# Kernel tuning notes

Hardware: AMD Instinct MI355X
Metric: run time of the kernel (lower is better)

Reference implementation:

```python
import jax, jax.numpy as jnp
import numpy as np

N = 20000; E = 240000; F_IN = 128; EMB = 256; H = 2
G = 128; DENSE = 512; NCLS = 10; NL = 3; SLOPE = 0.2  # PyG GATConv default negative_slope

def setup_inputs() -> dict:
    key = jax.random.key(0)
    ks = jax.random.split(key, 64); it = iter(ks)
    def rn(shape, s=0.05):
        return jax.random.normal(next(it), shape, jnp.float32) * s
    inp = {}
    inp["x"] = jax.random.normal(next(it), (N, F_IN), jnp.float32)
    inp["edge_index"] = jax.random.randint(next(it), (2, E), 0, N)
    inp["batch_index"] = jnp.sort(jax.random.randint(next(it), (N,), 0, G))
    for i in range(NL):
        fin = F_IN if i == 0 else EMB
        inp[f"att_W{i}"] = rn((fin, H * EMB))
        inp[f"att_asrc{i}"] = rn((H, EMB))
        inp[f"att_adst{i}"] = rn((H, EMB))
        inp[f"att_b{i}"] = rn((H * EMB,))
        inp[f"lin_W{i}"] = rn((H * EMB, EMB))
        inp[f"lin_b{i}"] = rn((EMB,))
    inp["line1_W"] = rn((2 * EMB, DENSE))
    inp["line1_b"] = rn((DENSE,))
    inp["line2_W"] = rn((DENSE, NCLS))
    inp["line2_b"] = rn((NCLS,))
    return inp

def _gat_conv(x, src, dst, W, a_src, a_dst, b):
    # PyG GATConv, heads=2, concat=True, self-loops already in (src,dst)
    h = (x @ W).reshape(N, H, EMB)                     # [N,H,C]
    al_src = jnp.sum(h * a_src[None], -1)              # [N,H]
    al_dst = jnp.sum(h * a_dst[None], -1)              # [N,H]
    e = jax.nn.leaky_relu(al_src[src] + al_dst[dst], SLOPE)  # [Etot,H]
    m = jax.ops.segment_max(e, dst, num_segments=N)    # segment softmax over incoming edges
    ex = jnp.exp(e - m[dst])
    s = jax.ops.segment_sum(ex, dst, num_segments=N)
    alpha = ex / s[dst]
    out = jax.ops.segment_sum(h[src] * alpha[:, :, None], dst, num_segments=N)
    return out.reshape(N, H * EMB) + b

def _pool(x, batch_index):
    counts = jax.ops.segment_sum(jnp.ones((N,), x.dtype), batch_index, num_segments=G)
    mean = jax.ops.segment_sum(x, batch_index, num_segments=G) / jnp.maximum(counts, 1.0)[:, None]
    mx = jax.ops.segment_max(x, batch_index, num_segments=G)
    mx = jnp.where(counts[:, None] > 0, mx, 0.0)
    return jnp.concatenate([mx, mean], axis=1)         # [G, 2*EMB]

def _forward(x, edge_index, batch_index, params):
    loop = jnp.arange(N)
    src = jnp.concatenate([edge_index[0], loop])       # GATConv adds self-loops
    dst = jnp.concatenate([edge_index[1], loop])
    reps = []
    for i in range(NL):
        W, asrc, adst, b, lW, lb = params[i]
        x = jax.nn.relu(_gat_conv(x, src, dst, W, asrc, adst, b))
        x = jax.nn.relu(x @ lW + lb)
        reps.append(_pool(x, batch_index))
    g = reps[0] + reps[1] + reps[2]
    line1_W, line1_b, line2_W, line2_b = params[NL]
    g = jax.nn.relu(g @ line1_W + line1_b)
    # dropout is identity in eval mode
    return g @ line2_W + line2_b

def reference(x, edge_index, batch_index, att_W0, att_asrc0, att_adst0, att_b0, lin_W0, lin_b0, att_W1, att_asrc1, att_adst1, att_b1, lin_W1, lin_b1, att_W2, att_asrc2, att_adst2, att_b2, lin_W2, lin_b2, line1_W, line1_b, line2_W, line2_b):
    params = [
        (att_W0, att_asrc0, att_adst0, att_b0, lin_W0, lin_b0),
        (att_W1, att_asrc1, att_adst1, att_b1, lin_W1, lin_b1),
        (att_W2, att_asrc2, att_adst2, att_b2, lin_W2, lin_b2),
        (line1_W, line1_b, line2_W, line2_b),
    ]
    return _forward(x, edge_index, batch_index, params)
```

## Files before the change

### kernel.cpp

```cpp
#include <hip/hip_runtime.h>

#define Nn 20000
#define Ee 240000
#define ET (Ee + Nn)
#define EMB 256
#define HE  512
#define NG  128
#define DENSE 512
#define NCLS 10
#define SLOPE 0.2f
#define NB 79
#define PS 8

typedef unsigned short u16;
typedef short bf16x8 __attribute__((ext_vector_type(8)));
typedef float f32x4 __attribute__((ext_vector_type(4)));

__device__ __forceinline__ u16 f2bf(float f) {
    unsigned u = __float_as_uint(f);
    unsigned r = (u + 0x7fffu + ((u >> 16) & 1u)) >> 16;
    return (u16)r;
}
__device__ __forceinline__ float bf2f(u16 u) {
    return __uint_as_float(((unsigned)u) << 16);
}

__device__ __forceinline__ float wave_sum(float v) {
#pragma unroll
    for (int off = 32; off > 0; off >>= 1) v += __shfl_down(v, off, 64);
    return v;
}
__device__ __forceinline__ float block_sum4(float v, volatile float* red4) {
    v = wave_sum(v);
    if ((threadIdx.x & 63) == 0) red4[threadIdx.x >> 6] = v;
    __syncthreads();
    float r = red4[0] + red4[1] + red4[2] + red4[3];
    __syncthreads();
    return r;
}

__global__ __launch_bounds__(256) void conv_bf16_zero(const float* __restrict__ in, u16* __restrict__ out,
                                                      int n4, int* __restrict__ deg,
                                                      float* __restrict__ poolbuf) {
    if (blockIdx.x < NB) {
        int z = blockIdx.x * 256 + threadIdx.x;
        if (z < Nn) deg[z] = 0;
    }
    if (blockIdx.x >= 1000 && blockIdx.x < 1512) {
        int z = (blockIdx.x - 1000) * 256 + threadIdx.x;
        poolbuf[z] = 0.f;
    }
    int i = blockIdx.x * 256 + threadIdx.x;
    if (i >= n4) return;
    float4 v = ((const float4*)in)[i];
    ushort4 o;
    o.x = f2bf(v.x); o.y = f2bf(v.y); o.z = f2bf(v.z); o.w = f2bf(v.w);
    ((ushort4*)out)[i] = o;
}

struct PrepArgs {
    const float* attW[3]; const float* linW[3];
    const float* asrc[3]; const float* adst[3];
    u16* wt1[3]; u16* wt2[3]; float* wvec;
    int fin[3];
};

__global__ __launch_bounds__(256) void prep_weights(PrepArgs a) {
    __shared__ float tile[32][33];
    int task = blockIdx.y, bx = blockIdx.x, t = threadIdx.x;
    if (task < 3) {
        int i = task, K = a.fin[i];
        int nb = bx & 15, kb = bx >> 4;
        if (kb * 32 >= K) return;
        int n0 = nb * 32, k0 = kb * 32;
        int tx = t & 31, ty = t >> 5;
        const float* in = a.attW[i];
        u16* out = a.wt1[i];
#pragma unroll
        for (int j = 0; j < 32; j += 8) tile[ty + j][tx] = in[(size_t)(k0 + ty + j) * 512 + n0 + tx];
        __syncthreads();
#pragma unroll
        for (int j = 0; j < 32; j += 8) out[(size_t)(n0 + ty + j) * K + k0 + tx] = f2bf(tile[tx][ty + j]);
    } else if (task < 6) {
        int i = task - 3;
        int nb = bx & 7, kb = bx >> 3;
        if (kb >= 16) return;
        int n0 = nb * 32, k0 = kb * 32;
        int tx = t & 31, ty = t >> 5;
        const float* in = a.linW[i];
        u16* out = a.wt2[i];
#pragma unroll
        for (int j = 0; j < 32; j += 8) tile[ty + j][tx] = in[(size_t)(k0 + ty + j) * 256 + n0 + tx];
        __syncthreads();
#pragma unroll
        for (int j = 0; j < 32; j += 8) out[(size_t)(n0 + ty + j) * 512 + k0 + tx] = f2bf(tile[tx][ty + j]);
    } else {
        int i = task - 6, k = bx;
        if (k >= a.fin[i]) return;
        volatile float* red4 = &tile[0][0];
        const float* W = a.attW[i];
        float w0 = W[(size_t)k * HE + t];
        float w1 = W[(size_t)k * HE + EMB + t];
        float s0 = block_sum4(w0 * a.asrc[i][t], red4);
        float s1 = block_sum4(w1 * a.asrc[i][EMB + t], red4);
        float d0 = block_sum4(w0 * a.adst[i][t], red4);
        float d1 = block_sum4(w1 * a.adst[i][EMB + t], red4);
        if (t == 0) {
            float* wv = a.wvec + i * 1024 + k * 4;
            wv[0] = s0; wv[1] = s1; wv[2] = d0; wv[3] = d1;
        }
    }
}

__global__ __launch_bounds__(256) void edge_hist(const int* __restrict__ ei, int* __restrict__ deg) {
    int e = blockIdx.x * 256 + threadIdx.x;
    if (e >= ET) return;
    int d = (e < Ee) ? ei[Ee + e] : (e - Ee);
    atomicAdd(&deg[d], 1);
}

__global__ __launch_bounds__(256) void scan_blocks(const int* __restrict__ deg, int* __restrict__ incl,
                                                   int* __restrict__ bsum) {
    __shared__ int buf[256];
    int i = blockIdx.x * 256 + threadIdx.x;
    int v = (i < Nn) ? deg[i] : 0;
    buf[threadIdx.x] = v;
    __syncthreads();
    for (int off = 1; off < 256; off <<= 1) {
        int add = (threadIdx.x >= off) ? buf[threadIdx.x - off] : 0;
        __syncthreads();
        buf[threadIdx.x] += add;
        __syncthreads();
    }
    if (i < Nn) incl[i] = buf[threadIdx.x];
    if (threadIdx.x == 255) bsum[blockIdx.x] = buf[255];
}

__global__ __launch_bounds__(256) void scan_tops_groups(const int* __restrict__ bsum, int* __restrict__ boff,
                                                        const int* __restrict__ batch, int* __restrict__ gptr) {
    if (blockIdx.x == 0) {
        __shared__ int buf[128];
        int t = threadIdx.x;
        if (t < 128) buf[t] = (t < NB) ? bsum[t] : 0;
        __syncthreads();
        for (int off = 1; off < 128; off <<= 1) {
            int add = 0;
            if (t < 128 && t >= off) add = buf[t - off];
            __syncthreads();
            if (t < 128) buf[t] += add;
            __syncthreads();
        }
        if (t < NB) boff[t] = (t == 0) ? 0 : buf[t - 1];
    } else {
        int g = threadIdx.x;
        if (g > NG) return;
        int lo = 0, hi = Nn;
        while (lo < hi) {
            int mid = (lo + hi) >> 1;
            if (batch[mid] < g) lo = mid + 1; else hi = mid;
        }
        gptr[g] = lo;
    }
}

__global__ __launch_bounds__(256) void scan_add_cursor(const int* __restrict__ incl, const int* __restrict__ boff,
                                                       const int* __restrict__ deg, int* __restrict__ rowptr,
                                                       int* __restrict__ cursor) {
    int i = blockIdx.x * 256 + threadIdx.x;
    if (i < Nn) {
        int inc = incl[i] + boff[blockIdx.x];
        rowptr[i + 1] = inc;
        cursor[i] = inc - deg[i];
    }
    if (i == 0) rowptr[0] = 0;
}

__global__ __launch_bounds__(256) void edge_scatter(const int* __restrict__ ei, int* __restrict__ cursor,
                                                    int* __restrict__ colv) {
    int e = blockIdx.x * 256 + threadIdx.x;
    if (e >= ET) return;
    int s, d;
    if (e < Ee) { s = ei[e]; d = ei[Ee + e]; }
    else        { s = d = e - Ee; }
    int pos = atomicAdd(&cursor[d], 1);
    colv[pos] = s;
}

#define GL_LDS(gsrc, ldst)                                                               \
    __builtin_amdgcn_global_load_lds(                                                    \
        (const __attribute__((address_space(1))) void*)(unsigned long long)(gsrc),       \
        (__attribute__((address_space(3))) void*)(unsigned)(unsigned long long)(ldst),   \
        16, 0, 0)

__global__ __launch_bounds__(256) void gemm_bf16(const u16* __restrict__ A, int lda, int aoff,
                                                 const u16* __restrict__ Bt, const float* __restrict__ bias,
                                                 u16* __restrict__ Cb, int M, int N, int K, int relu) {
    __shared__ alignas(16) char sA[8192];
    __shared__ alignas(16) char sB[8192];
    int tid = threadIdx.x, lane = tid & 63, wid = tid >> 6;
    int l15 = lane & 15, q = lane >> 4;
    int row0 = blockIdx.y * 128, col0 = blockIdx.x * 128;
    int wrow = (wid >> 1) * 64, wcol = (wid & 1) * 64;
    int ao = (col0 >= 256) ? aoff : 0;

    f32x4 acc[4][4];
#pragma unroll
    for (int m = 0; m < 4; m++)
#pragma unroll
        for (int n = 0; n < 4; n++)
#pragma unroll
            for (int e = 0; e < 4; e++) acc[m][n][e] = 0.f;

    for (int k0 = 0; k0 < K; k0 += 32) {
#pragma unroll
        for (int is = 0; is < 2; ++is) {
            int base = is * 4096 + wid * 1024;
            int o = base + lane * 16;
            int row = o >> 6, kb = o & 63;
            int gr = row0 + row; gr = gr < M ? gr : M - 1;
            const char* src = (const char*)(A + (size_t)gr * lda + ao + k0) + kb;
            GL_LDS(src, sA + base);
        }
#pragma unroll
        for (int is = 0; is < 2; ++is) {
            int base = is * 4096 + wid * 1024;
            int o = base + lane * 16;
            int row = o >> 6, kb = o & 63;
            const char* src = (const char*)(Bt + (size_t)(col0 + row) * K + k0) + kb;
            GL_LDS(src, sB + base);
        }
        __syncthreads();

        bf16x8 af[4], bfr[4];
#pragma unroll
        for (int m = 0; m < 4; m++)
            af[m] = *(const bf16x8*)(sA + ((wrow + m * 16 + l15) << 6) + q * 16);
#pragma unroll
        for (int n = 0; n < 4; n++)
            bfr[n] = *(const bf16x8*)(sB + ((wcol + n * 16 + l15) << 6) + q * 16);
#pragma unroll
        for (int m = 0; m < 4; m++)
#pragma unroll
            for (int n = 0; n < 4; n++)
                acc[m][n] = __builtin_amdgcn_mfma_f32_16x16x32_bf16(af[m], bfr[n], acc[m][n], 0, 0, 0);
        __syncthreads();
    }

#pragma unroll
    for (int m = 0; m < 4; m++) {
        int rbase = row0 + wrow + m * 16 + q * 4;
#pragma unroll
        for (int reg = 0; reg < 4; reg++) {
            int r = rbase + reg;
            if (r >= M) continue;
#pragma unroll
            for (int n = 0; n < 4; n++) {
                int c = col0 + wcol + n * 16 + l15;
                float v = acc[m][n][reg] + (bias ? bias[c] : 0.f);
                if (relu) v = fmaxf(v, 0.f);
                Cb[(size_t)r * N + c] = f2bf(v);
            }
        }
    }
}

__global__ __launch_bounds__(256) void compute_al_fused(const u16* __restrict__ Xb, const float* __restrict__ wvec,
                                                        float* __restrict__ alsrc, float* __restrict__ aldst,
                                                        int fin) {
    int n = blockIdx.x * 4 + (threadIdx.x >> 6);
    int lane = threadIdx.x & 63;
    float s0 = 0.f, s1 = 0.f, d0 = 0.f, d1 = 0.f;
    for (int j = lane; j < fin; j += 64) {
        float x = bf2f(Xb[(size_t)n * fin + j]);
        float4 w = *(const float4*)(wvec + j * 4);
        s0 += x * w.x; s1 += x * w.y; d0 += x * w.z; d1 += x * w.w;
    }
#pragma unroll
    for (int off = 32; off > 0; off >>= 1) {
        s0 += __shfl_xor(s0, off, 64); s1 += __shfl_xor(s1, off, 64);
        d0 += __shfl_xor(d0, off, 64); d1 += __shfl_xor(d1, off, 64);
    }
    if (lane == 0) {
        alsrc[n * 2 + 0] = s0; alsrc[n * 2 + 1] = s1;
        aldst[n * 2 + 0] = d0; aldst[n * 2 + 1] = d1;
    }
}

__device__ __forceinline__ float lrelu(float x) { return x >= 0.f ? x : SLOPE * x; }

template <int FIN>
__global__ __launch_bounds__(256) void attn_agg_x(const u16* __restrict__ Xb,
                                                  const float* __restrict__ alsrc,
                                                  const float* __restrict__ aldst,
                                                  const int* __restrict__ row_ptr,
                                                  const int* __restrict__ colv,
                                                  u16* __restrict__ Zb) {
    constexpr int FPL = FIN / 64;
    int d = blockIdx.x * 4 + (threadIdx.x >> 6);
    int lane = threadIdx.x & 63;
    float ad0 = aldst[d * 2 + 0], ad1 = aldst[d * 2 + 1];
    int beg = row_ptr[d], end = row_ptr[d + 1];
    float S0 = 0.f, S1 = 0.f;
    float a0[FPL] = {}, a1[FPL] = {};

    int k = beg;
    for (; k + 3 < end; k += 4) {
        int ss[4];
        float e0[4], e1[4];
        u16 vv[4][FPL];
#pragma unroll
        for (int u = 0; u < 4; u++) ss[u] = colv[k + u];
#pragma unroll
        for (int u = 0; u < 4; u++) {
            float2 l = *(const float2*)(alsrc + ss[u] * 2);
            e0[u] = __expf(lrelu(l.x + ad0));
            e1[u] = __expf(lrelu(l.y + ad1));
            if constexpr (FPL == 4)
                *(ushort4*)vv[u] = *(const ushort4*)(Xb + (size_t)ss[u] * FIN + lane * 4);
            else
                *(ushort2*)vv[u] = *(const ushort2*)(Xb + (size_t)ss[u] * FIN + lane * 2);
        }
#pragma unroll
        for (int u = 0; u < 4; u++) {
            S0 += e0[u]; S1 += e1[u];
#pragma unroll
            for (int j = 0; j < FPL; j++) {
                float x = bf2f(vv[u][j]);
                a0[j] += e0[u] * x;
                a1[j] += e1[u] * x;
            }
        }
    }
    for (; k < end; ++k) {
        int s0 = colv[k];
        float2 l0 = *(const float2*)(alsrc + s0 * 2);
        float e00 = __expf(lrelu(l0.x + ad0)), e01 = __expf(lrelu(l0.y + ad1));
        u16 v0[FPL];
        if constexpr (FPL == 4) *(ushort4*)v0 = *(const ushort4*)(Xb + (size_t)s0 * FIN + lane * 4);
        else                    *(ushort2*)v0 = *(const ushort2*)(Xb + (size_t)s0 * FIN + lane * 2);
        S0 += e00; S1 += e01;
#pragma unroll
        for (int j = 0; j < FPL; j++) {
            float x0 = bf2f(v0[j]);
            a0[j] += e00 * x0;
            a1[j] += e01 * x0;
        }
    }

    float r0 = 1.f / S0, r1 = 1.f / S1;
    u16 o0[FPL], o1[FPL];
#pragma unroll
    for (int j = 0; j < FPL; j++) { o0[j] = f2bf(a0[j] * r0); o1[j] = f2bf(a1[j] * r1); }
    u16* q = Zb + (size_t)d * (2 * FIN);
    if constexpr (FPL == 4) {
        *(ushort4*)(q + lane * 4)       = *(ushort4*)o0;
        *(ushort4*)(q + FIN + lane * 4) = *(ushort4*)o1;
    } else {
        *(ushort2*)(q + lane * 2)       = *(ushort2*)o0;
        *(ushort2*)(q + FIN + lane * 2) = *(ushort2*)o1;
    }
}

__global__ __launch_bounds__(256) void pool_atomic(const u16* __restrict__ Xb, const int* __restrict__ gptr,
                                                   float* __restrict__ pmax, float* __restrict__ psum) {
    int g = blockIdx.x, sb = blockIdx.y, t = threadIdx.x;
    int beg = gptr[g], end = gptr[g + 1];
    float mx = 0.f, sm = 0.f;
    for (int n = beg + sb; n < end; n += PS) {
        float v = bf2f(Xb[(size_t)n * EMB + t]);
        mx = fmaxf(mx, v);
        sm += v;
    }
    atomicMax((int*)&pmax[g * EMB + t], __float_as_int(mx));
    atomicAdd(&psum[g * EMB + t], sm);
}

__global__ __launch_bounds__(256) void head1(const float* __restrict__ pmax3, const float* __restrict__ psum,
                                             const int* __restrict__ gptr,
                                             const float* __restrict__ l1W, const float* __restrict__ l1b,
                                             float* __restrict__ g1) {
    __shared__ float row[512];
    __shared__ float part[256];
    int r = blockIdx.y, t = threadIdx.x;
    for (int j = t; j < 512; j += 256) {
        float v;
        if (j < EMB) {
            v = pmax3[r * EMB + j] + pmax3[32768 + r * EMB + j] + pmax3[65536 + r * EMB + j];
        } else {
            int cnt = gptr[r + 1] - gptr[r];
            v = psum[r * EMB + (j - EMB)] / fmaxf((float)cnt, 1.f);
        }
        row[j] = v;
    }
    __syncthreads();
    int cl = t & 63, kq = t >> 6;
    int c = blockIdx.x * 64 + cl;
    int k0 = kq * 128;
    float acc = 0.f;
#pragma unroll 8
    for (int k = 0; k < 128; k++) acc += row[k0 + k] * l1W[(size_t)(k0 + k) * DENSE + c];
    part[t] = acc;
    __syncthreads();
    if (kq == 0) {
        float v = part[cl] + part[64 + cl] + part[128 + cl] + part[192 + cl];
        g1[(size_t)r * DENSE + c] = fmaxf(v + l1b[c], 0.f);
    }
}

__global__ __launch_bounds__(64) void line2_kernel(const float* __restrict__ g1, const float* __restrict__ W,
                                                   const float* __restrict__ b, float* __restrict__ out) {
    int r = blockIdx.x, t = threadIdx.x;
    float acc[NCLS] = {};
    for (int k = t; k < 2 * EMB; k += 64) {
        float gv = g1[r * 512 + k];
#pragma unroll
        for (int c = 0; c < NCLS; c++) acc[c] += gv * W[k * NCLS + c];
    }
#pragma unroll
    for (int c = 0; c < NCLS; c++) {
        float v = acc[c];
#pragma unroll
        for (int off = 32; off > 0; off >>= 1) v += __shfl_down(v, off, 64);
        if (t == 0) out[r * NCLS + c] = v + b[c];
    }
}

extern "C" void kernel_launch(void* const* d_in, const int* in_sizes, int n_in,
                              void* d_out, int out_size, void* d_ws, size_t ws_size,
                              hipStream_t stream) {
    const float* x_in  = (const float*)d_in[0];
    const int*   ei    = (const int*)d_in[1];
    const int*   batch = (const int*)d_in[2];
    const float* attW[3] = {(const float*)d_in[3],  (const float*)d_in[9],  (const float*)d_in[15]};
    const float* asrc[3] = {(const float*)d_in[4],  (const float*)d_in[10], (const float*)d_in[16]};
    const float* adst[3] = {(const float*)d_in[5],  (const float*)d_in[11], (const float*)d_in[17]};
    const float* attB[3] = {(const float*)d_in[6],  (const float*)d_in[12], (const float*)d_in[18]};
    const float* linW[3] = {(const float*)d_in[7],  (const float*)d_in[13], (const float*)d_in[19]};
    const float* linB[3] = {(const float*)d_in[8],  (const float*)d_in[14], (const float*)d_in[20]};
    const float* l1W = (const float*)d_in[21];
    const float* l1b = (const float*)d_in[22];
    const float* l2W = (const float*)d_in[23];
    const float* l2b = (const float*)d_in[24];
    float* out = (float*)d_out;

    char* ws = (char*)d_ws;
    size_t off = 0;
    auto alloc = [&](size_t bytes) -> void* {
        void* p = ws + off;
        off += (bytes + 255) & ~(size_t)255;
        return p;
    };
    u16*   Zb     = (u16*)alloc((size_t)Nn * HE * 2);
    u16*   Xb     = (u16*)alloc((size_t)Nn * EMB * 2);
    u16*   Yb     = (u16*)alloc((size_t)Nn * HE * 2);
    u16*   wt1[3], *wt2[3];
    for (int i = 0; i < 3; i++) {
        wt1[i] = (u16*)alloc((size_t)512 * 512 * 2);
        wt2[i] = (u16*)alloc((size_t)256 * 512 * 2);
    }
    float* wvec   = (float*)alloc((size_t)3 * 256 * 4 * 4);
    float* alsrc  = (float*)alloc((size_t)Nn * 2 * 4);
    float* aldst  = (float*)alloc((size_t)Nn * 2 * 4);
    int*   deg    = (int*)alloc((size_t)Nn * 4);
    int*   incl   = (int*)alloc((size_t)Nn * 4);
    int*   bsum   = (int*)alloc((size_t)NB * 4);
    int*   boff   = (int*)alloc((size_t)NB * 4);
    int*   rowptr = (int*)alloc((size_t)(Nn + 1) * 4);
    int*   cursor = (int*)alloc((size_t)Nn * 4);
    int*   colv   = (int*)alloc((size_t)ET * 4);
    int*   gptr   = (int*)alloc((size_t)(NG + 1) * 4);
    float* poolbuf = (float*)alloc((size_t)(3 * NG * EMB + NG * EMB) * 4);
    float* pmax3  = poolbuf;
    float* psumA  = poolbuf + 3 * NG * EMB;
    float* g1     = (float*)alloc((size_t)NG * DENSE * 4);

    conv_bf16_zero<<<(Nn * 128 / 4 + 255) / 256, 256, 0, stream>>>(x_in, Xb, Nn * 128 / 4, deg, poolbuf);

    PrepArgs pa;
    for (int i = 0; i < 3; i++) {
        pa.attW[i] = attW[i]; pa.linW[i] = linW[i];
        pa.asrc[i] = asrc[i]; pa.adst[i] = adst[i];
        pa.wt1[i] = wt1[i];   pa.wt2[i] = wt2[i];
        pa.fin[i] = (i == 0) ? 128 : EMB;
    }
    pa.wvec = wvec;
    prep_weights<<<dim3(256, 9), 256, 0, stream>>>(pa);

    edge_hist<<<(ET + 255) / 256, 256, 0, stream>>>(ei, deg);
    scan_blocks<<<NB, 256, 0, stream>>>(deg, incl, bsum);
    scan_tops_groups<<<2, 256, 0, stream>>>(bsum, boff, batch, gptr);
    scan_add_cursor<<<NB, 256, 0, stream>>>(incl, boff, deg, rowptr, cursor);
    edge_scatter<<<(ET + 255) / 256, 256, 0, stream>>>(ei, cursor, colv);

    for (int i = 0; i < 3; i++) {
        int fin = (i == 0) ? 128 : EMB;
        compute_al_fused<<<Nn / 4, 256, 0, stream>>>(Xb, wvec + i * 1024, alsrc, aldst, fin);
        if (fin == 128)
            attn_agg_x<128><<<Nn / 4, 256, 0, stream>>>(Xb, alsrc, aldst, rowptr, colv, Zb);
        else
            attn_agg_x<256><<<Nn / 4, 256, 0, stream>>>(Xb, alsrc, aldst, rowptr, colv, Zb);
        gemm_bf16<<<dim3(512 / 128, (Nn + 127) / 128), 256, 0, stream>>>(
            Zb, 2 * fin, fin, wt1[i], attB[i], Yb, Nn, 512, fin, 1);
        gemm_bf16<<<dim3(256 / 128, (Nn + 127) / 128), 256, 0, stream>>>(
            Yb, 512, 0, wt2[i], linB[i], Xb, Nn, 256, 512, 1);
        pool_atomic<<<dim3(NG, PS), 256, 0, stream>>>(Xb, gptr, pmax3 + i * NG * EMB, psumA);
    }

    head1<<<dim3(8, NG), 256, 0, stream>>>(pmax3, psumA, gptr, l1W, l1b, g1);
    line2_kernel<<<NG, 64, 0, stream>>>(g1, l2W, l2b, out);
}
```

Before: 420.0 us.

## Merge prologue kernels, fuse pooling with next-layer attention logits, deepen GEMM K-tile

```diff
diff --git a/kernel.cpp b/kernel.cpp
--- a/kernel.cpp
+++ b/kernel.cpp
@@ -39,25 +39,6 @@
     return r;
 }
 
-__global__ __launch_bounds__(256) void conv_bf16_zero(const float* __restrict__ in, u16* __restrict__ out,
-                                                      int n4, int* __restrict__ deg,
-                                                      float* __restrict__ poolbuf) {
-    if (blockIdx.x < NB) {
-        int z = blockIdx.x * 256 + threadIdx.x;
-        if (z < Nn) deg[z] = 0;
-    }
-    if (blockIdx.x >= 1000 && blockIdx.x < 1512) {
-        int z = (blockIdx.x - 1000) * 256 + threadIdx.x;
-        poolbuf[z] = 0.f;
-    }
-    int i = blockIdx.x * 256 + threadIdx.x;
-    if (i >= n4) return;
-    float4 v = ((const float4*)in)[i];
-    ushort4 o;
-    o.x = f2bf(v.x); o.y = f2bf(v.y); o.z = f2bf(v.z); o.w = f2bf(v.w);
-    ((ushort4*)out)[i] = o;
-}
-
 struct PrepArgs {
     const float* attW[3]; const float* linW[3];
     const float* asrc[3]; const float* adst[3];
@@ -65,10 +46,31 @@
     int fin[3];
 };
 
-__global__ __launch_bounds__(256) void prep_weights(PrepArgs a) {
+__global__ __launch_bounds__(256) void prologue_all(const float* __restrict__ xin, u16* __restrict__ Xb,
+                                                    int n4, int* __restrict__ deg, float* __restrict__ poolbuf,
+                                                    PrepArgs a) {
     __shared__ float tile[32][33];
-    int task = blockIdx.y, bx = blockIdx.x, t = threadIdx.x;
+    int t = threadIdx.x, bx = blockIdx.x, y = blockIdx.y;
+    if (y == 0) {
+        if (bx < NB) {
+            int z = bx * 256 + t;
+            if (z < Nn) deg[z] = 0;
+        }
+        if (bx >= 1000 && bx < 1512) {
+            int z = (bx - 1000) * 256 + t;
+            poolbuf[z] = 0.f;
+        }
+        int i = bx * 256 + t;
+        if (i >= n4) return;
+        float4 v = ((const float4*)xin)[i];
+        ushort4 o;
+        o.x = f2bf(v.x); o.y = f2bf(v.y); o.z = f2bf(v.z); o.w = f2bf(v.w);
+        ((ushort4*)Xb)[i] = o;
+        return;
+    }
+    int task = y - 1;
     if (task < 3) {
+        if (bx >= 256) return;
         int i = task, K = a.fin[i];
         int nb = bx & 15, kb = bx >> 4;
         if (kb * 32 >= K) return;
@@ -82,6 +84,7 @@
 #pragma unroll
         for (int j = 0; j < 32; j += 8) out[(size_t)(n0 + ty + j) * K + k0 + tx] = f2bf(tile[tx][ty + j]);
     } else if (task < 6) {
+        if (bx >= 128) return;
         int i = task - 3;
         int nb = bx & 7, kb = bx >> 3;
         if (kb >= 16) return;
@@ -195,8 +198,8 @@
 __global__ __launch_bounds__(256) void gemm_bf16(const u16* __restrict__ A, int lda, int aoff,
                                                  const u16* __restrict__ Bt, const float* __restrict__ bias,
                                                  u16* __restrict__ Cb, int M, int N, int K, int relu) {
-    __shared__ alignas(16) char sA[8192];
-    __shared__ alignas(16) char sB[8192];
+    __shared__ alignas(16) char sA[16384];
+    __shared__ alignas(16) char sB[16384];
     int tid = threadIdx.x, lane = tid & 63, wid = tid >> 6;
     int l15 = lane & 15, q = lane >> 4;
     int row0 = blockIdx.y * 128, col0 = blockIdx.x * 128;
@@ -211,38 +214,41 @@
 #pragma unroll
             for (int e = 0; e < 4; e++) acc[m][n][e] = 0.f;
 
-    for (int k0 = 0; k0 < K; k0 += 32) {
-#pragma unroll
-        for (int is = 0; is < 2; ++is) {
+    for (int k0 = 0; k0 < K; k0 += 64) {
+#pragma unroll
+        for (int is = 0; is < 4; ++is) {
             int base = is * 4096 + wid * 1024;
             int o = base + lane * 16;
-            int row = o >> 6, kb = o & 63;
+            int row = (o >> 6) & 127, ks = o >> 13, kb = o & 63;
             int gr = row0 + row; gr = gr < M ? gr : M - 1;
-            const char* src = (const char*)(A + (size_t)gr * lda + ao + k0) + kb;
+            const char* src = (const char*)(A + (size_t)gr * lda + ao + k0) + ks * 64 + kb;
             GL_LDS(src, sA + base);
         }
 #pragma unroll
-        for (int is = 0; is < 2; ++is) {
+        for (int is = 0; is < 4; ++is) {
             int base = is * 4096 + wid * 1024;
             int o = base + lane * 16;
-            int row = o >> 6, kb = o & 63;
-            const char* src = (const char*)(Bt + (size_t)(col0 + row) * K + k0) + kb;
+            int row = (o >> 6) & 127, ks = o >> 13, kb = o & 63;
+            const char* src = (const char*)(Bt + (size_t)(col0 + row) * K + k0) + ks * 64 + kb;
             GL_LDS(src, sB + base);
         }
         __syncthreads();
 
-        bf16x8 af[4], bfr[4];
-#pragma unroll
-        for (int m = 0; m < 4; m++)
-            af[m] = *(const bf16x8*)(sA + ((wrow + m * 16 + l15) << 6) + q * 16);
-#pragma unroll
-        for (int n = 0; n < 4; n++)
-            bfr[n] = *(const bf16x8*)(sB + ((wcol + n * 16 + l15) << 6) + q * 16);
-#pragma unroll
-        for (int m = 0; m < 4; m++)
+#pragma unroll
+        for (int ks = 0; ks < 2; ks++) {
+            bf16x8 af[4], bfr[4];
+#pragma unroll
+            for (int m = 0; m < 4; m++)
+                af[m] = *(const bf16x8*)(sA + ks * 8192 + ((wrow + m * 16 + l15) << 6) + q * 16);
 #pragma unroll
             for (int n = 0; n < 4; n++)
-                acc[m][n] = __builtin_amdgcn_mfma_f32_16x16x32_bf16(af[m], bfr[n], acc[m][n], 0, 0, 0);
+                bfr[n] = *(const bf16x8*)(sB + ks * 8192 + ((wcol + n * 16 + l15) << 6) + q * 16);
+#pragma unroll
+            for (int m = 0; m < 4; m++)
+#pragma unroll
+                for (int n = 0; n < 4; n++)
+                    acc[m][n] = __builtin_amdgcn_mfma_f32_16x16x32_bf16(af[m], bfr[n], acc[m][n], 0, 0, 0);
+        }
         __syncthreads();
     }
 
@@ -361,18 +367,43 @@
     }
 }
 
-__global__ __launch_bounds__(256) void pool_atomic(const u16* __restrict__ Xb, const int* __restrict__ gptr,
-                                                   float* __restrict__ pmax, float* __restrict__ psum) {
-    int g = blockIdx.x, sb = blockIdx.y, t = threadIdx.x;
-    int beg = gptr[g], end = gptr[g + 1];
-    float mx = 0.f, sm = 0.f;
-    for (int n = beg + sb; n < end; n += PS) {
-        float v = bf2f(Xb[(size_t)n * EMB + t]);
-        mx = fmaxf(mx, v);
-        sm += v;
-    }
-    atomicMax((int*)&pmax[g * EMB + t], __float_as_int(mx));
-    atomicAdd(&psum[g * EMB + t], sm);
+__global__ __launch_bounds__(256) void pool_al(const u16* __restrict__ Xb, const int* __restrict__ gptr,
+                                               float* __restrict__ pmax, float* __restrict__ psum,
+                                               const float* __restrict__ wvec,
+                                               float* __restrict__ alsrc, float* __restrict__ aldst) {
+    int bx = blockIdx.x, t = threadIdx.x;
+    if (bx < 1024) {
+        int g = bx >> 3, sb = bx & 7;
+        int beg = gptr[g], end = gptr[g + 1];
+        float mx = 0.f, sm = 0.f;
+        for (int n = beg + sb; n < end; n += PS) {
+            float v = bf2f(Xb[(size_t)n * EMB + t]);
+            mx = fmaxf(mx, v);
+            sm += v;
+        }
+        atomicMax((int*)&pmax[g * EMB + t], __float_as_int(mx));
+        atomicAdd(&psum[g * EMB + t], sm);
+    } else {
+        int n = (bx - 1024) * 4 + (t >> 6);
+        int lane = t & 63;
+        float s0 = 0.f, s1 = 0.f, d0 = 0.f, d1 = 0.f;
+#pragma unroll
+        for (int jj = 0; jj < 4; jj++) {
+            int j = lane + jj * 64;
+            float x = bf2f(Xb[(size_t)n * EMB + j]);
+            float4 w = *(const float4*)(wvec + j * 4);
+            s0 += x * w.x; s1 += x * w.y; d0 += x * w.z; d1 += x * w.w;
+        }
+#pragma unroll
+        for (int off = 32; off > 0; off >>= 1) {
+            s0 += __shfl_xor(s0, off, 64); s1 += __shfl_xor(s1, off, 64);
+            d0 += __shfl_xor(d0, off, 64); d1 += __shfl_xor(d1, off, 64);
+        }
+        if (lane == 0) {
+            alsrc[n * 2 + 0] = s0; alsrc[n * 2 + 1] = s1;
+            aldst[n * 2 + 0] = d0; aldst[n * 2 + 1] = d1;
+        }
+    }
 }
 
 __global__ __launch_bounds__(256) void head1(const float* __restrict__ pmax3, const float* __restrict__ psum,
@@ -474,8 +505,6 @@
     float* psumA  = poolbuf + 3 * NG * EMB;
     float* g1     = (float*)alloc((size_t)NG * DENSE * 4);
 
-    conv_bf16_zero<<<(Nn * 128 / 4 + 255) / 256, 256, 0, stream>>>(x_in, Xb, Nn * 128 / 4, deg, poolbuf);
-
     PrepArgs pa;
     for (int i = 0; i < 3; i++) {
         pa.attW[i] = attW[i]; pa.linW[i] = linW[i];
@@ -484,7 +513,7 @@
         pa.fin[i] = (i == 0) ? 128 : EMB;
     }
     pa.wvec = wvec;
-    prep_weights<<<dim3(256, 9), 256, 0, stream>>>(pa);
+    prologue_all<<<dim3(2500, 10), 256, 0, stream>>>(x_in, Xb, Nn * 128 / 4, deg, poolbuf, pa);
 
     edge_hist<<<(ET + 255) / 256, 256, 0, stream>>>(ei, deg);
     scan_blocks<<<NB, 256, 0, stream>>>(deg, incl, bsum);
@@ -492,9 +521,10 @@
     scan_add_cursor<<<NB, 256, 0, stream>>>(incl, boff, deg, rowptr, cursor);
     edge_scatter<<<(ET + 255) / 256, 256, 0, stream>>>(ei, cursor, colv);
 
+    compute_al_fused<<<Nn / 4, 256, 0, stream>>>(Xb, wvec, alsrc, aldst, 128);
+
     for (int i = 0; i < 3; i++) {
         int fin = (i == 0) ? 128 : EMB;
-        compute_al_fused<<<Nn / 4, 256, 0, stream>>>(Xb, wvec + i * 1024, alsrc, aldst, fin);
         if (fin == 128)
             attn_agg_x<128><<<Nn / 4, 256, 0, stream>>>(Xb, alsrc, aldst, rowptr, colv, Zb);
         else
@@ -503,7 +533,9 @@
             Zb, 2 * fin, fin, wt1[i], attB[i], Yb, Nn, 512, fin, 1);
         gemm_bf16<<<dim3(256 / 128, (Nn + 127) / 128), 256, 0, stream>>>(
             Yb, 512, 0, wt2[i], linB[i], Xb, Nn, 256, 512, 1);
-        pool_atomic<<<dim3(NG, PS), 256, 0, stream>>>(Xb, gptr, pmax3 + i * NG * EMB, psumA);
+        int nblk = (i < 2) ? (1024 + Nn / 4) : 1024;
+        pool_al<<<nblk, 256, 0, stream>>>(Xb, gptr, pmax3 + i * NG * EMB, psumA,
+                                          wvec + (i + 1) * 1024, alsrc, aldst);
     }
 
     head1<<<dim3(8, NG), 256, 0, stream>>>(pmax3, psumA, gptr, l1W, l1b, g1);
```

Measured after the change: 404.4 us. 1.04x faster.
